# Performance work log

Hardware: AMD Instinct MI355X
Metric: run time of the kernel (lower is better)

## Reference

```python
import jax, jax.numpy as jnp
import numpy as np

B, N, U = 8, 2048, 256
BN_EPS = 1e-3  # keras BatchNormalization default epsilon
ADJ_DENSITY = 0.008  # ~16 neighbors per node on average


def setup_inputs() -> dict:
    key = jax.random.key(0)
    ks = jax.random.split(key, 16)
    s = 0.05  # weight scale ('random_normal' init is small-stddev in keras)
    x = jax.random.normal(ks[0], (B, N, U), jnp.float32)
    # sparse binary adjacency stored dense (per-sample SpMM pattern)
    adj = (jax.random.uniform(ks[1], (B, N, N)) < ADJ_DENSITY).astype(jnp.float32)
    nodal_mask = jnp.ones((B, N), jnp.float32)
    return {
        'x': x, 'adj': adj, 'nodal_mask': nodal_mask,
        'W_lin': jax.random.normal(ks[2], (U, U)) * s, 'b_lin': jnp.zeros((U,)),
        'Wq_mp': jax.random.normal(ks[3], (3, U, U)) * s, 'bq_mp': jnp.zeros((3, U)),
        'Wk_mp': jax.random.normal(ks[4], (3, U, U)) * s, 'bk_mp': jnp.zeros((3, U)),
        'Wv_mp': jax.random.normal(ks[5], (3, U, U)) * s, 'bv_mp': jnp.zeros((3, U)),
        'Wk_att': jax.random.normal(ks[6], (U, U)) * s,
        'Wv_att': jax.random.normal(ks[7], (U, U)) * s,
        'Wq_att': jax.random.normal(ks[8], (U, U)) * s,
        'Wo_att': jax.random.normal(ks[9], (U, U)) * s,
        'bn_gamma': jnp.ones((U,)), 'bn_beta': jnp.zeros((U,)),
        'bn_mean': jnp.zeros((U,)), 'bn_var': jnp.ones((U,)),
        'W_proj': jax.random.normal(ks[10], (U, U)) * s, 'b_proj': jnp.zeros((U,)),
        'W_res': jax.random.normal(ks[11], (U, U)) * s, 'b_res': jnp.zeros((U,)),
    }


def _dympn(x, adj, Ws, bs, mask):
    # 3 message-passing layers, each applied K_l=2 times (inference value)
    for i in range(3):
        for _ in range(2):
            xn = jnp.einsum('bmn,bnd->bmd', adj, x)  # batched SpMM (graph_conv mode)
            x = jax.nn.silu(jnp.einsum('bmd,de->bme', xn, Ws[i]) + bs[i])
    return x * mask[:, :, None]


def reference(x, adj, nodal_mask, W_lin, b_lin, Wq_mp, bq_mp, Wk_mp, bk_mp,
              Wv_mp, bv_mp, Wk_att, Wv_att, Wq_att, Wo_att,
              bn_gamma, bn_beta, bn_mean, bn_var, W_proj, b_proj, W_res, b_res):
    initial_x = x
    adj = jax.lax.stop_gradient(adj)
    h = jnp.einsum('bnd,de->bne', x, W_lin) + b_lin
    q = _dympn(h, adj, Wq_mp, bq_mp, nodal_mask)
    k = _dympn(h, adj, Wk_mp, bk_mp, nodal_mask)
    v = _dympn(h, adj, Wv_mp, bv_mp, nodal_mask)
    # linear attention
    m = nodal_mask[:, :, None]
    pk = jax.nn.silu(jnp.einsum('bnd,de->bne', k, Wk_att) * m)
    pv = jnp.einsum('bnd,de->bne', v, Wv_att) * m
    pq = jnp.einsum('bnd,de->bne', q, Wq_att)
    kv = jnp.einsum('bnd,bne->bde', pk, pv)       # [B,U,U]
    attn = jnp.einsum('bnd,bde->bne', pq, kv)
    attn = jnp.einsum('bnd,de->bne', attn, Wo_att)
    # batch norm (inference: moving stats) over last axis
    y = attn + initial_x
    y = bn_gamma * (y - bn_mean) * jax.lax.rsqrt(bn_var + BN_EPS) + bn_beta
    out = jax.nn.silu(jnp.einsum('bnd,de->bne', y, W_proj) + b_proj)
    out = out + jnp.einsum('bnd,de->bne', initial_x, W_res) + b_res
    out = out * nodal_mask[:, :, None]
    return out
```

## Files before the change

kernel.cpp:

```cpp
#include <hip/hip_runtime.h>
#include <stdint.h>

#define NB 8
#define NN 2048
#define NU 256
#define CAP 64
#define BNEPS 0.001f

typedef __attribute__((ext_vector_type(8))) short short8;
typedef __attribute__((ext_vector_type(4))) float floatx4;
typedef unsigned short u16;
typedef unsigned int u32;

__device__ __forceinline__ float bf2f(u16 u) {
  union { u32 i; float f; } c; c.i = ((u32)u) << 16; return c.f;
}
__device__ __forceinline__ u16 f2bf(float f) {
  union { float f; u32 i; } c; c.f = f;
  return (u16)((c.i + 0x7fffu + ((c.i >> 16) & 1u)) >> 16);
}
__device__ __forceinline__ void splitbf(float a, u16& h, u16& l) {
  h = f2bf(a);
  l = f2bf(a - bf2f(h));
}

enum : unsigned {
  F_BIAS = 2u, F_SILU = 4u, F_MASKPRE = 8u, F_MASKPOST = 16u,
  F_ADDX = 32u, F_BN = 64u, F_ADDT = 128u, F_BPERMAT = 512u,
  F_TPLANES = 1024u, F_OUTHL = 2048u
};

#define TP_MAT 524288
#define TP_LO  4194304
#define MSZ ((size_t)NN * NU)

__global__ __launch_bounds__(256) void build_nbr_k(
    const float* __restrict__ adj, int* __restrict__ cnt, int* __restrict__ idx)
{
  int row = blockIdx.x;
  const float* base = adj + (size_t)row * NN;
  __shared__ int c;
  if (threadIdx.x == 0) c = 0;
  __syncthreads();
#pragma unroll
  for (int j = 0; j < 8; j++) {
    int n = j * 256 + threadIdx.x;
    if (base[n] != 0.f) {
      int p = atomicAdd(&c, 1);
      if (p < CAP) idx[(size_t)row * CAP + p] = n;
    }
  }
  __syncthreads();
  if (threadIdx.x == 0) cnt[row] = (c < CAP ? c : CAP);
}

struct WPtrs { const float* p[16]; };

__global__ __launch_bounds__(256) void conv_w_k(WPtrs wp, u16* __restrict__ dst)
{
  int gid = blockIdx.x * 256 + threadIdx.x;
  int mat = gid >> 13;
  int rem = gid & 8191;
  int kb = rem >> 10;
  int n = (rem >> 2) & 255;
  int slot = rem & 3;
  int qv = (slot - (n >> 1)) & 3;
  int k0 = kb * 32 + qv * 8;
  const float* W = wp.p[mat];
  u32 oh[4], ol[4];
#pragma unroll
  for (int t2 = 0; t2 < 4; t2++) {
    float f0 = W[(size_t)(k0 + 2 * t2) * 256 + n];
    float f1 = W[(size_t)(k0 + 2 * t2 + 1) * 256 + n];
    u16 h0, l0, h1, l1;
    splitbf(f0, h0, l0);
    splitbf(f1, h1, l1);
    oh[t2] = (u32)h0 | ((u32)h1 << 16);
    ol[t2] = (u32)l0 | ((u32)l1 << 16);
  }
  uint4 qh; qh.x = oh[0]; qh.y = oh[1]; qh.z = oh[2]; qh.w = oh[3];
  uint4 ql; ql.x = ol[0]; ql.y = ol[1]; ql.z = ol[2]; ql.w = ol[3];
  *(uint4*)(dst + (size_t)gid * 8) = qh;
  *(uint4*)(dst + 1048576 + (size_t)gid * 8) = ql;
}

__global__ __launch_bounds__(256) void conv_x_k(
    const float* __restrict__ x, u16* __restrict__ dst, size_t oLo)
{
  size_t i = ((size_t)blockIdx.x * 256 + threadIdx.x) * 4;
  float4 v = *(const float4*)(x + i);
  u16 h0, l0, h1, l1, h2, l2, h3, l3;
  splitbf(v.x, h0, l0); splitbf(v.y, h1, l1);
  splitbf(v.z, h2, l2); splitbf(v.w, h3, l3);
  uint2 H; H.x = (u32)h0 | ((u32)h1 << 16); H.y = (u32)h2 | ((u32)h3 << 16);
  uint2 L; L.x = (u32)l0 | ((u32)l1 << 16); L.y = (u32)l2 | ((u32)l3 << 16);
  *(uint2*)(dst + i) = H;
  *(uint2*)(dst + oLo + i) = L;
}

template <unsigned F>
__device__ __forceinline__ void gemm_epi(
    floatx4 (&acc)[4][2], int b, int bm, int w, int m16, int q,
    const float* __restrict__ bias, const float* __restrict__ mask,
    const float* __restrict__ xf32,
    const float* __restrict__ gma, const float* __restrict__ bta,
    const float* __restrict__ bmu, const float* __restrict__ bvr,
    const float* __restrict__ addt, void* __restrict__ outp, size_t oLo)
{
#pragma unroll
  for (int mt = 0; mt < 4; mt++) {
    if (F & F_TPLANES) {
      u16* oh = (u16*)outp + (size_t)b * TP_MAT;
      u16* ol = oh + TP_LO;
      int gr0 = bm + mt * 16 + q * 4;
#pragma unroll
      for (int nt = 0; nt < 2; nt++) {
        int col = w * 32 + nt * 16 + m16;
        u16 hh[4], ll[4];
#pragma unroll
        for (int r = 0; r < 4; r++) {
          float t2 = acc[mt][nt][r];
          float mv = mask[b * NN + gr0 + r];
          if (F & F_MASKPRE) t2 *= mv;
          if (F & F_SILU) t2 = t2 / (1.f + __expf(-t2));
          if (F & F_MASKPOST) t2 *= mv;
          splitbf(t2, hh[r], ll[r]);
        }
        uint2 H2, L2v;
        H2.x = (u32)hh[0] | ((u32)hh[1] << 16);
        H2.y = (u32)hh[2] | ((u32)hh[3] << 16);
        L2v.x = (u32)ll[0] | ((u32)ll[1] << 16);
        L2v.y = (u32)ll[2] | ((u32)ll[3] << 16);
        *(uint2*)(oh + (size_t)col * 2048 + gr0) = H2;
        *(uint2*)(ol + (size_t)col * 2048 + gr0) = L2v;
      }
    } else {
#pragma unroll
      for (int r = 0; r < 4; r++) {
        int gr = bm + mt * 16 + q * 4 + r;
        float mval = 1.f;
        if (F & (F_MASKPRE | F_MASKPOST)) mval = mask[b * NN + gr];
#pragma unroll
        for (int nt = 0; nt < 2; nt++) {
          int col = w * 32 + nt * 16 + m16;
          float t2 = acc[mt][nt][r];
          if (F & F_BIAS) t2 += bias[col];
          if (F & F_MASKPRE) t2 *= mval;
          if (F & F_SILU) t2 = t2 / (1.f + __expf(-t2));
          if (F & F_ADDX) t2 += xf32[((size_t)b * NN + gr) * NU + col];
          if (F & F_BN) t2 = gma[col] * (t2 - bmu[col]) * rsqrtf(bvr[col] + BNEPS) + bta[col];
          if (F & F_ADDT) t2 += addt[((size_t)b * NN + gr) * NU + col];
          if (F & F_MASKPOST) t2 *= mval;
          size_t o = ((size_t)b * NN + gr) * NU + col;
          if (F & F_OUTHL) {
            u16 h0, l0;
            splitbf(t2, h0, l0);
            ((u16*)outp)[o] = h0;
            ((u16*)outp)[o + oLo] = l0;
          } else {
            ((float*)outp)[o] = t2;
          }
        }
      }
    }
  }
}

template <int NG, unsigned F0, unsigned F1, unsigned F2>
__global__ __launch_bounds__(512, 4) void gemm_k(
    const u16* __restrict__ A0, const u16* __restrict__ A1, const u16* __restrict__ A2,
    size_t aLo,
    const u16* __restrict__ W0, const u16* __restrict__ W1, const u16* __restrict__ W2,
    size_t wLo,
    const float* __restrict__ b0, const float* __restrict__ b1, const float* __restrict__ b2,
    const float* __restrict__ mask,
    const float* __restrict__ xf32,
    const float* __restrict__ gma, const float* __restrict__ bta,
    const float* __restrict__ bmu, const float* __restrict__ bvr,
    const float* __restrict__ addt,
    void* __restrict__ o0, void* __restrict__ o1, void* __restrict__ o2,
    size_t oLo)
{
  const int tid = threadIdx.x;
  const int id = blockIdx.x;
  const int xcd = id & 7;
  const int t = id >> 3;
  const int chain = (NG == 1) ? 0 : (t % NG);
  const int xt = (NG == 1) ? t : (t / NG);
  const int b = xcd;
  const int bm = xt * 64;

  __shared__ alignas(16) u16 Ah[64 * 264];
  __shared__ alignas(16) u16 Al[64 * 264];

  const u16* Abase = (chain == 0) ? A0 : (chain == 1 ? A1 : A2);
  const u16* Wsel = (chain == 0) ? W0 : (chain == 1 ? W1 : W2);
  if (F0 & F_BPERMAT) Wsel = W0 + (size_t)b * 65536;
  const u16* Whi = Wsel;
  const u16* Wlo = Whi + wLo;
  const u16* Ahp = Abase + (size_t)b * MSZ;
  const u16* Alp = Ahp + aLo;

#pragma unroll
  for (int s = tid; s < 1024; s += 512) {
    int r = s >> 4;
    int c = (s & 15) << 4;
    size_t ao = (size_t)(bm + r) * 256 + c;
    *(uint4*)&Ah[r * 264 + c] = *(const uint4*)(Ahp + ao);
    *(uint4*)&Ah[r * 264 + c + 8] = *(const uint4*)(Ahp + ao + 8);
    *(uint4*)&Al[r * 264 + c] = *(const uint4*)(Alp + ao);
    *(uint4*)&Al[r * 264 + c + 8] = *(const uint4*)(Alp + ao + 8);
  }
  __syncthreads();

  const int lane = tid & 63;
  const int w = tid >> 6;
  const int m16 = lane & 15;
  const int q = lane >> 4;

  floatx4 acc[4][2];
#pragma unroll
  for (int i = 0; i < 4; i++)
#pragma unroll
    for (int j = 0; j < 2; j++) acc[i][j] = (floatx4){0.f, 0.f, 0.f, 0.f};

#pragma unroll
  for (int kk = 0; kk < 8; kk++) {
    short8 bh[2], bl2[2];
#pragma unroll
    for (int nt = 0; nt < 2; nt++) {
      int n = w * 32 + nt * 16 + m16;
      size_t off = (size_t)kk * 8192 + (size_t)n * 32 + (size_t)(((q + (n >> 1)) & 3) * 8);
      bh[nt] = *(const short8*)(Whi + off);
      bl2[nt] = *(const short8*)(Wlo + off);
    }
#pragma unroll
    for (int mt = 0; mt < 4; mt++) {
      int row = mt * 16 + m16;
      short8 ah = *(const short8*)&Ah[row * 264 + kk * 32 + q * 8];
      short8 al2 = *(const short8*)&Al[row * 264 + kk * 32 + q * 8];
#pragma unroll
      for (int nt = 0; nt < 2; nt++) {
        acc[mt][nt] = __builtin_amdgcn_mfma_f32_16x16x32_bf16(ah, bh[nt], acc[mt][nt], 0, 0, 0);
        acc[mt][nt] = __builtin_amdgcn_mfma_f32_16x16x32_bf16(al2, bh[nt], acc[mt][nt], 0, 0, 0);
        acc[mt][nt] = __builtin_amdgcn_mfma_f32_16x16x32_bf16(ah, bl2[nt], acc[mt][nt], 0, 0, 0);
      }
    }
  }

  if (NG == 1 || chain == 0)
    gemm_epi<F0>(acc, b, bm, w, m16, q, b0, mask, xf32, gma, bta, bmu, bvr, addt, o0, oLo);
  else if (chain == 1)
    gemm_epi<F1>(acc, b, bm, w, m16, q, b1, mask, xf32, gma, bta, bmu, bvr, addt, o1, oLo);
  else
    gemm_epi<F2>(acc, b, bm, w, m16, q, b2, mask, xf32, gma, bta, bmu, bvr, addt, o2, oLo);
}

template <unsigned F>
__global__ __launch_bounds__(256, 8) void agg_k(
    const float* __restrict__ g, u16* __restrict__ xo, size_t oLo,
    const float* __restrict__ bq, const float* __restrict__ bk, const float* __restrict__ bv,
    const float* __restrict__ mask,
    const int* __restrict__ ncnt, const int* __restrict__ nidx)
{
  int id = blockIdx.x;
  int c3 = id >> 12;
  int sub = id & 4095;
  int b = sub & 7;
  int rg = sub >> 3;
  int tid = threadIdx.x;
  int w = tid >> 6;
  int l = tid & 63;
  int row = rg * 4 + w;
  int rowid = b * NN + row;
  const float* __restrict__ gm = g + ((size_t)c3 * 8 + b) * MSZ;
  const float* bias = (c3 == 0) ? bq : (c3 == 1 ? bk : bv);
  int cnt = ncnt[rowid];
  const int* __restrict__ ip = nidx + (size_t)rowid * CAP;
  int c = l * 4;
  float4 a; a.x = a.y = a.z = a.w = 0.f;
  int e = 0;
  for (; e + 4 <= cnt; e += 4) {
    int4 i4 = *(const int4*)(ip + e);
    float4 v0 = *(const float4*)(gm + ((size_t)i4.x << 8) + c);
    float4 v1 = *(const float4*)(gm + ((size_t)i4.y << 8) + c);
    float4 v2 = *(const float4*)(gm + ((size_t)i4.z << 8) + c);
    float4 v3 = *(const float4*)(gm + ((size_t)i4.w << 8) + c);
    a.x += v0.x + v1.x + v2.x + v3.x;
    a.y += v0.y + v1.y + v2.y + v3.y;
    a.z += v0.z + v1.z + v2.z + v3.z;
    a.w += v0.w + v1.w + v2.w + v3.w;
  }
  for (; e < cnt; e++) {
    float4 v = *(const float4*)(gm + ((size_t)ip[e] << 8) + c);
    a.x += v.x; a.y += v.y; a.z += v.z; a.w += v.w;
  }
  float4 bb = *(const float4*)(bias + c);
  float o[4] = {a.x + bb.x, a.y + bb.y, a.z + bb.z, a.w + bb.w};
  float mv = (F & F_MASKPOST) ? mask[rowid] : 1.f;
  u16 hh[4], ll[4];
#pragma unroll
  for (int j = 0; j < 4; j++) {
    float t = o[j];
    if (F & F_SILU) t = t / (1.f + __expf(-t));
    if (F & F_MASKPOST) t *= mv;
    splitbf(t, hh[j], ll[j]);
  }
  uint2 H; H.x = (u32)hh[0] | ((u32)hh[1] << 16); H.y = (u32)hh[2] | ((u32)hh[3] << 16);
  uint2 L; L.x = (u32)ll[0] | ((u32)ll[1] << 16); L.y = (u32)ll[2] | ((u32)ll[3] << 16);
  size_t o0 = ((size_t)c3 * 8 + b) * MSZ + ((size_t)row << 8) + c;
  *(uint2*)(xo + o0) = H;
  *(uint2*)(xo + oLo + o0) = L;
}

__global__ __launch_bounds__(256, 2) void kv_k(
    const u16* __restrict__ pkT, const u16* __restrict__ pvT, float* __restrict__ part)
{
  int et = blockIdx.x * 128;
  int dt = blockIdx.y * 128;
  int z = blockIdx.z;
  int b = z & 7;
  int p = z >> 3;
  int tid = threadIdx.x;
  int lane = tid & 63, w = tid >> 6;
  int m16 = lane & 15, q = lane >> 4;

  const u16* pkh = pkT + (size_t)b * TP_MAT;
  const u16* pkl = pkh + TP_LO;
  const u16* pvh = pvT + (size_t)b * TP_MAT;
  const u16* pvl = pvh + TP_LO;

  int d_base = dt + (w >> 1) * 64 + m16;
  int e_base = et + (w & 1) * 64 + m16;

  floatx4 acc[4][4];
#pragma unroll
  for (int i = 0; i < 4; i++)
#pragma unroll
    for (int j = 0; j < 4; j++) acc[i][j] = (floatx4){0.f, 0.f, 0.f, 0.f};

#pragma unroll
  for (int kt = 0; kt < 8; kt++) {
    int kc = p * 256 + kt * 32 + q * 8;
    short8 ah[4], al[4], bh[4], bl[4];
#pragma unroll
    for (int mt = 0; mt < 4; mt++) {
      size_t o = (size_t)(d_base + mt * 16) * 2048 + kc;
      ah[mt] = *(const short8*)(pkh + o);
      al[mt] = *(const short8*)(pkl + o);
    }
#pragma unroll
    for (int nt = 0; nt < 4; nt++) {
      size_t o = (size_t)(e_base + nt * 16) * 2048 + kc;
      bh[nt] = *(const short8*)(pvh + o);
      bl[nt] = *(const short8*)(pvl + o);
    }
#pragma unroll
    for (int mt = 0; mt < 4; mt++)
#pragma unroll
      for (int nt = 0; nt < 4; nt++) {
        acc[mt][nt] = __builtin_amdgcn_mfma_f32_16x16x32_bf16(ah[mt], bh[nt], acc[mt][nt], 0, 0, 0);
        acc[mt][nt] = __builtin_amdgcn_mfma_f32_16x16x32_bf16(al[mt], bh[nt], acc[mt][nt], 0, 0, 0);
        acc[mt][nt] = __builtin_amdgcn_mfma_f32_16x16x32_bf16(ah[mt], bl[nt], acc[mt][nt], 0, 0, 0);
      }
  }

#pragma unroll
  for (int mt = 0; mt < 4; mt++)
#pragma unroll
    for (int r = 0; r < 4; r++) {
      int d = dt + (w >> 1) * 64 + mt * 16 + q * 4 + r;
#pragma unroll
      for (int nt = 0; nt < 4; nt++) {
        int e = et + (w & 1) * 64 + nt * 16 + m16;
        part[(size_t)z * 65536 + (size_t)d * 256 + e] = acc[mt][nt][r];
      }
    }
}

__global__ __launch_bounds__(256) void kv_conv_k(const float* __restrict__ part, u16* __restrict__ dst)
{
  int gid = blockIdx.x * 256 + threadIdx.x;
  int b = gid >> 13;
  int rem = gid & 8191;
  int kb = rem >> 10;
  int e = (rem >> 2) & 255;
  int slot = rem & 3;
  int qv = (slot - (e >> 1)) & 3;
  int d0 = kb * 32 + qv * 8;
  const float* src = part + (size_t)b * 65536 + (size_t)d0 * 256 + e;
  u32 oh[4], ol[4];
#pragma unroll
  for (int t2 = 0; t2 < 4; t2++) {
    float s0 = 0.f, s1 = 0.f;
#pragma unroll
    for (int pp = 0; pp < 8; pp++) {
      const float* sp = src + (size_t)pp * 524288 + t2 * 512;
      s0 += sp[0];
      s1 += sp[256];
    }
    u16 h0, l0, h1, l1;
    splitbf(s0, h0, l0);
    splitbf(s1, h1, l1);
    oh[t2] = (u32)h0 | ((u32)h1 << 16);
    ol[t2] = (u32)l0 | ((u32)l1 << 16);
  }
  uint4 qh; qh.x = oh[0]; qh.y = oh[1]; qh.z = oh[2]; qh.w = oh[3];
  uint4 ql; ql.x = ol[0]; ql.y = ol[1]; ql.z = ol[2]; ql.w = ol[3];
  *(uint4*)(dst + (size_t)gid * 8) = qh;
  *(uint4*)(dst + 524288 + (size_t)gid * 8) = ql;
}

extern "C" void kernel_launch(void* const* d_in, const int* in_sizes, int n_in,
                              void* d_out, int out_size, void* d_ws, size_t ws_size,
                              hipStream_t stream)
{
  const float* x = (const float*)d_in[0];
  const float* adj = (const float*)d_in[1];
  const float* mask = (const float*)d_in[2];
  const float* W_lin = (const float*)d_in[3];
  const float* b_lin = (const float*)d_in[4];
  const float* Wq_mp = (const float*)d_in[5];
  const float* bq_mp = (const float*)d_in[6];
  const float* Wk_mp = (const float*)d_in[7];
  const float* bk_mp = (const float*)d_in[8];
  const float* Wv_mp = (const float*)d_in[9];
  const float* bv_mp = (const float*)d_in[10];
  const float* Wk_att = (const float*)d_in[11];
  const float* Wv_att = (const float*)d_in[12];
  const float* Wq_att = (const float*)d_in[13];
  const float* Wo_att = (const float*)d_in[14];
  const float* bn_gamma = (const float*)d_in[15];
  const float* bn_beta = (const float*)d_in[16];
  const float* bn_mean = (const float*)d_in[17];
  const float* bn_var = (const float*)d_in[18];
  const float* W_proj = (const float*)d_in[19];
  const float* b_proj = (const float*)d_in[20];
  const float* W_res = (const float*)d_in[21];
  const float* b_res = (const float*)d_in[22];

  char* ws = (char*)d_ws;
  int* CNT    = (int*)(ws + 0);
  int* IDX    = (int*)(ws + (1ull << 20));
  u16* WSZ    = (u16*)(ws + (5ull << 20));
  u16* KVS    = (u16*)(ws + (9ull << 20));
  float* KVP  = (float*)(ws + (11ull << 20));
  u16* XHL    = (u16*)(ws + (27ull << 20));
  u16* HHL    = (u16*)(ws + (43ull << 20));
  float* G    = (float*)(ws + (59ull << 20));
  u16* XA     = (u16*)(ws + (107ull << 20));
  u16* XB     = (u16*)(ws + (155ull << 20));

  const size_t WLO = 1048576;
  const size_t KLO = 524288;
  const size_t A8  = 8 * MSZ;
  const size_t A24 = 24 * MSZ;

  u16* PQHL = HHL;
  u16* PKT = (u16*)G;
  u16* PVT = (u16*)((char*)G + (16ull << 20));
  u16* ATT = (u16*)((char*)G + (32ull << 20));
  u16* YHL = XA;
  float* TMP = (float*)((char*)XA + (16ull << 20));

  WPtrs wp;
  wp.p[0] = W_lin;
  wp.p[1] = Wq_mp; wp.p[2] = Wq_mp + 65536; wp.p[3] = Wq_mp + 131072;
  wp.p[4] = Wk_mp; wp.p[5] = Wk_mp + 65536; wp.p[6] = Wk_mp + 131072;
  wp.p[7] = Wv_mp; wp.p[8] = Wv_mp + 65536; wp.p[9] = Wv_mp + 131072;
  wp.p[10] = Wk_att; wp.p[11] = Wv_att; wp.p[12] = Wq_att; wp.p[13] = Wo_att;
  wp.p[14] = W_proj; wp.p[15] = W_res;
  conv_w_k<<<512, 256, 0, stream>>>(wp, WSZ);
  conv_x_k<<<4096, 256, 0, stream>>>(x, XHL, A8);
  build_nbr_k<<<NB * NN, 256, 0, stream>>>(adj, CNT, IDX);

  gemm_k<1, F_BIAS | F_OUTHL, 0u, 0u><<<256, 512, 0, stream>>>(
      XHL, XHL, XHL, A8, WSZ, WSZ, WSZ, WLO,
      b_lin, nullptr, nullptr, mask, nullptr,
      bn_gamma, bn_beta, bn_mean, bn_var, nullptr,
      HHL, nullptr, nullptr, A8);

  u16* xbufs[2] = {XA, XB};
  for (int s = 0; s < 6; s++) {
    int i = s >> 1;
    const u16* Wq_s = WSZ + (size_t)(1 + i) * 65536;
    const u16* Wk_s = WSZ + (size_t)(4 + i) * 65536;
    const u16* Wv_s = WSZ + (size_t)(7 + i) * 65536;
    u16* inb = (s == 0) ? HHL : xbufs[(s + 1) & 1];
    size_t aLo = (s == 0) ? A8 : A24;
    const u16* Aq = inb;
    const u16* Ak = (s == 0) ? inb : inb + 8 * MSZ;
    const u16* Av = (s == 0) ? inb : inb + 16 * MSZ;
    u16* ob = xbufs[s & 1];
    gemm_k<3, 0u, 0u, 0u><<<768, 512, 0, stream>>>(
        Aq, Ak, Av, aLo, Wq_s, Wk_s, Wv_s, WLO,
        nullptr, nullptr, nullptr, mask, nullptr,
        bn_gamma, bn_beta, bn_mean, bn_var, nullptr,
        G, G + 8 * MSZ, G + 16 * MSZ, 0);
    const float* bq = bq_mp + i * 256;
    const float* bk = bk_mp + i * 256;
    const float* bv = bv_mp + i * 256;
    if (s == 5)
      agg_k<F_BIAS | F_SILU | F_MASKPOST><<<12288, 256, 0, stream>>>(
          G, ob, A24, bq, bk, bv, mask, CNT, IDX);
    else
      agg_k<F_BIAS | F_SILU><<<12288, 256, 0, stream>>>(
          G, ob, A24, bq, bk, bv, mask, CNT, IDX);
  }

  gemm_k<3, F_OUTHL, F_SILU | F_MASKPRE | F_TPLANES, F_MASKPOST | F_TPLANES>
      <<<768, 512, 0, stream>>>(
      XB, XB + 8 * MSZ, XB + 16 * MSZ, A24,
      WSZ + (size_t)12 * 65536, WSZ + (size_t)10 * 65536, WSZ + (size_t)11 * 65536, WLO,
      nullptr, nullptr, nullptr, mask, nullptr,
      bn_gamma, bn_beta, bn_mean, bn_var, nullptr,
      PQHL, PKT, PVT, A8);

  kv_k<<<dim3(2, 2, 64), 256, 0, stream>>>(PKT, PVT, KVP);
  kv_conv_k<<<256, 256, 0, stream>>>(KVP, KVS);

  gemm_k<1, F_BPERMAT | F_OUTHL, 0u, 0u><<<256, 512, 0, stream>>>(
      PQHL, PQHL, PQHL, A8, KVS, KVS, KVS, KLO,
      nullptr, nullptr, nullptr, mask, nullptr,
      bn_gamma, bn_beta, bn_mean, bn_var, nullptr,
      ATT, nullptr, nullptr, A8);

  gemm_k<1, F_ADDX | F_BN | F_OUTHL, 0u, 0u><<<256, 512, 0, stream>>>(
      ATT, ATT, ATT, A8,
      WSZ + (size_t)13 * 65536, nullptr, nullptr, WLO,
      nullptr, nullptr, nullptr, mask, x,
      bn_gamma, bn_beta, bn_mean, bn_var, nullptr,
      YHL, nullptr, nullptr, A8);

  gemm_k<1, F_BIAS, 0u, 0u><<<256, 512, 0, stream>>>(
      XHL, XHL, XHL, A8,
      WSZ + (size_t)15 * 65536, nullptr, nullptr, WLO,
      b_res, nullptr, nullptr, mask, nullptr,
      bn_gamma, bn_beta, bn_mean, bn_var, nullptr,
      TMP, nullptr, nullptr, 0);

  gemm_k<1, F_BIAS | F_SILU | F_ADDT | F_MASKPOST, 0u, 0u><<<256, 512, 0, stream>>>(
      YHL, YHL, YHL, A8,
      WSZ + (size_t)14 * 65536, nullptr, nullptr, WLO,
      b_proj, nullptr, nullptr, mask, nullptr,
      bn_gamma, bn_beta, bn_mean, bn_var, TMP,
      d_out, nullptr, nullptr, 0);

  (void)in_sizes; (void)n_in; (void)out_size; (void)ws_size;
}
```

Before: 793.1 us.

## Fuse sparse neighbor aggregation into following GEMM prologue and merge setup kernels

Removes the separate agg_k kernel. Each GEMM now gathers the neighbor rows of the previous GEMM's fp32 output, adds bias, applies SiLU and mask, splits to bf16 hi/lo, and writes the result straight into shared memory as its A tile. This avoids writing and re-reading the intermediate bf16 hi/lo planes and saves six launches. The three setup kernels become one prologue kernel, and the chain index mapping changes to t>>5 so blocks of the same chain are grouped. The cost is that the gather now sits on the GEMM's critical path with fewer threads per row, which may leave the load latency exposed.

```diff
diff --git a/kernel.cpp b/kernel.cpp
--- a/kernel.cpp
+++ b/kernel.cpp
@@ -34,68 +34,67 @@
 #define TP_LO  4194304
 #define MSZ ((size_t)NN * NU)
 
-__global__ __launch_bounds__(256) void build_nbr_k(
+struct WPtrs { const float* p[16]; };
+
+__global__ __launch_bounds__(256) void prologue_k(
+    WPtrs wp, u16* __restrict__ wdst,
+    const float* __restrict__ x, u16* __restrict__ xdst, size_t xLo,
     const float* __restrict__ adj, int* __restrict__ cnt, int* __restrict__ idx)
 {
-  int row = blockIdx.x;
-  const float* base = adj + (size_t)row * NN;
-  __shared__ int c;
-  if (threadIdx.x == 0) c = 0;
-  __syncthreads();
-#pragma unroll
-  for (int j = 0; j < 8; j++) {
-    int n = j * 256 + threadIdx.x;
-    if (base[n] != 0.f) {
-      int p = atomicAdd(&c, 1);
-      if (p < CAP) idx[(size_t)row * CAP + p] = n;
-    }
-  }
-  __syncthreads();
-  if (threadIdx.x == 0) cnt[row] = (c < CAP ? c : CAP);
-}
-
-struct WPtrs { const float* p[16]; };
-
-__global__ __launch_bounds__(256) void conv_w_k(WPtrs wp, u16* __restrict__ dst)
-{
-  int gid = blockIdx.x * 256 + threadIdx.x;
-  int mat = gid >> 13;
-  int rem = gid & 8191;
-  int kb = rem >> 10;
-  int n = (rem >> 2) & 255;
-  int slot = rem & 3;
-  int qv = (slot - (n >> 1)) & 3;
-  int k0 = kb * 32 + qv * 8;
-  const float* W = wp.p[mat];
-  u32 oh[4], ol[4];
-#pragma unroll
-  for (int t2 = 0; t2 < 4; t2++) {
-    float f0 = W[(size_t)(k0 + 2 * t2) * 256 + n];
-    float f1 = W[(size_t)(k0 + 2 * t2 + 1) * 256 + n];
-    u16 h0, l0, h1, l1;
-    splitbf(f0, h0, l0);
-    splitbf(f1, h1, l1);
-    oh[t2] = (u32)h0 | ((u32)h1 << 16);
-    ol[t2] = (u32)l0 | ((u32)l1 << 16);
-  }
-  uint4 qh; qh.x = oh[0]; qh.y = oh[1]; qh.z = oh[2]; qh.w = oh[3];
-  uint4 ql; ql.x = ol[0]; ql.y = ol[1]; ql.z = ol[2]; ql.w = ol[3];
-  *(uint4*)(dst + (size_t)gid * 8) = qh;
-  *(uint4*)(dst + 1048576 + (size_t)gid * 8) = ql;
-}
-
-__global__ __launch_bounds__(256) void conv_x_k(
-    const float* __restrict__ x, u16* __restrict__ dst, size_t oLo)
-{
-  size_t i = ((size_t)blockIdx.x * 256 + threadIdx.x) * 4;
-  float4 v = *(const float4*)(x + i);
-  u16 h0, l0, h1, l1, h2, l2, h3, l3;
-  splitbf(v.x, h0, l0); splitbf(v.y, h1, l1);
-  splitbf(v.z, h2, l2); splitbf(v.w, h3, l3);
-  uint2 H; H.x = (u32)h0 | ((u32)h1 << 16); H.y = (u32)h2 | ((u32)h3 << 16);
-  uint2 L; L.x = (u32)l0 | ((u32)l1 << 16); L.y = (u32)l2 | ((u32)l3 << 16);
-  *(uint2*)(dst + i) = H;
-  *(uint2*)(dst + oLo + i) = L;
+  int bid = blockIdx.x;
+  int tid = threadIdx.x;
+  __shared__ int c0;
+  if (bid < 512) {
+    int gid = bid * 256 + tid;
+    int mat = gid >> 13;
+    int rem = gid & 8191;
+    int kb = rem >> 10;
+    int n = (rem >> 2) & 255;
+    int slot = rem & 3;
+    int qv = (slot - (n >> 1)) & 3;
+    int k0 = kb * 32 + qv * 8;
+    const float* W = wp.p[mat];
+    u32 oh[4], ol[4];
+#pragma unroll
+    for (int t2 = 0; t2 < 4; t2++) {
+      float f0 = W[(size_t)(k0 + 2 * t2) * 256 + n];
+      float f1 = W[(size_t)(k0 + 2 * t2 + 1) * 256 + n];
+      u16 h0, l0, h1, l1;
+      splitbf(f0, h0, l0);
+      splitbf(f1, h1, l1);
+      oh[t2] = (u32)h0 | ((u32)h1 << 16);
+      ol[t2] = (u32)l0 | ((u32)l1 << 16);
+    }
+    uint4 qh; qh.x = oh[0]; qh.y = oh[1]; qh.z = oh[2]; qh.w = oh[3];
+    uint4 ql; ql.x = ol[0]; ql.y = ol[1]; ql.z = ol[2]; ql.w = ol[3];
+    *(uint4*)(wdst + (size_t)gid * 8) = qh;
+    *(uint4*)(wdst + 1048576 + (size_t)gid * 8) = ql;
+  } else if (bid < 4608) {
+    size_t i = ((size_t)(bid - 512) * 256 + tid) * 4;
+    float4 v = *(const float4*)(x + i);
+    u16 h0, l0, h1, l1, h2, l2, h3, l3;
+    splitbf(v.x, h0, l0); splitbf(v.y, h1, l1);
+    splitbf(v.z, h2, l2); splitbf(v.w, h3, l3);
+    uint2 H; H.x = (u32)h0 | ((u32)h1 << 16); H.y = (u32)h2 | ((u32)h3 << 16);
+    uint2 L; L.x = (u32)l0 | ((u32)l1 << 16); L.y = (u32)l2 | ((u32)l3 << 16);
+    *(uint2*)(xdst + i) = H;
+    *(uint2*)(xdst + xLo + i) = L;
+  } else {
+    int row = bid - 4608;
+    const float* base = adj + (size_t)row * NN;
+    if (tid == 0) c0 = 0;
+    __syncthreads();
+#pragma unroll
+    for (int j = 0; j < 8; j++) {
+      int n = j * 256 + tid;
+      if (base[n] != 0.f) {
+        int p = atomicAdd(&c0, 1);
+        if (p < CAP) idx[(size_t)row * CAP + p] = n;
+      }
+    }
+    __syncthreads();
+    if (tid == 0) cnt[row] = (c0 < CAP ? c0 : CAP);
+  }
 }
 
 template <unsigned F>
@@ -166,7 +165,7 @@
   }
 }
 
-template <int NG, unsigned F0, unsigned F1, unsigned F2>
+template <int NG, unsigned SF, unsigned F0, unsigned F1, unsigned F2>
 __global__ __launch_bounds__(512, 4) void gemm_k(
     const u16* __restrict__ A0, const u16* __restrict__ A1, const u16* __restrict__ A2,
     size_t aLo,
@@ -179,37 +178,88 @@
     const float* __restrict__ bmu, const float* __restrict__ bvr,
     const float* __restrict__ addt,
     void* __restrict__ o0, void* __restrict__ o1, void* __restrict__ o2,
-    size_t oLo)
+    size_t oLo,
+    const float* __restrict__ gsrc,
+    const float* __restrict__ sb0, const float* __restrict__ sb1, const float* __restrict__ sb2,
+    const int* __restrict__ ncnt, const int* __restrict__ nidx)
 {
   const int tid = threadIdx.x;
   const int id = blockIdx.x;
   const int xcd = id & 7;
   const int t = id >> 3;
-  const int chain = (NG == 1) ? 0 : (t % NG);
-  const int xt = (NG == 1) ? t : (t / NG);
+  const int chain = (NG == 1) ? 0 : (t >> 5);
+  const int xt = (NG == 1) ? t : (t & 31);
   const int b = xcd;
   const int bm = xt * 64;
 
   __shared__ alignas(16) u16 Ah[64 * 264];
   __shared__ alignas(16) u16 Al[64 * 264];
 
-  const u16* Abase = (chain == 0) ? A0 : (chain == 1 ? A1 : A2);
   const u16* Wsel = (chain == 0) ? W0 : (chain == 1 ? W1 : W2);
   if (F0 & F_BPERMAT) Wsel = W0 + (size_t)b * 65536;
   const u16* Whi = Wsel;
   const u16* Wlo = Whi + wLo;
-  const u16* Ahp = Abase + (size_t)b * MSZ;
-  const u16* Alp = Ahp + aLo;
-
-#pragma unroll
-  for (int s = tid; s < 1024; s += 512) {
-    int r = s >> 4;
-    int c = (s & 15) << 4;
-    size_t ao = (size_t)(bm + r) * 256 + c;
-    *(uint4*)&Ah[r * 264 + c] = *(const uint4*)(Ahp + ao);
-    *(uint4*)&Ah[r * 264 + c + 8] = *(const uint4*)(Ahp + ao + 8);
-    *(uint4*)&Al[r * 264 + c] = *(const uint4*)(Alp + ao);
-    *(uint4*)&Al[r * 264 + c + 8] = *(const uint4*)(Alp + ao + 8);
+
+  if constexpr (SF != 0u) {
+    const int l = tid & 63;
+    const int wv = tid >> 6;
+    const float* __restrict__ gm = gsrc + ((size_t)chain * 8 + b) * MSZ;
+    const float* sb = (chain == 0) ? sb0 : (chain == 1 ? sb1 : sb2);
+    const int c = l * 4;
+    float4 bb = *(const float4*)(sb + c);
+#pragma unroll 1
+    for (int i = 0; i < 8; i++) {
+      const int r = wv * 8 + i;
+      const int gr = bm + r;
+      const int rowid = b * NN + gr;
+      const int cnt = ncnt[rowid];
+      const int* __restrict__ ip = nidx + (size_t)rowid * CAP;
+      float4 a; a.x = a.y = a.z = a.w = 0.f;
+      int e = 0;
+      for (; e + 4 <= cnt; e += 4) {
+        int4 i4 = *(const int4*)(ip + e);
+        float4 v0 = *(const float4*)(gm + ((size_t)i4.x << 8) + c);
+        float4 v1 = *(const float4*)(gm + ((size_t)i4.y << 8) + c);
+        float4 v2 = *(const float4*)(gm + ((size_t)i4.z << 8) + c);
+        float4 v3 = *(const float4*)(gm + ((size_t)i4.w << 8) + c);
+        a.x += v0.x + v1.x + v2.x + v3.x;
+        a.y += v0.y + v1.y + v2.y + v3.y;
+        a.z += v0.z + v1.z + v2.z + v3.z;
+        a.w += v0.w + v1.w + v2.w + v3.w;
+      }
+      for (; e < cnt; e++) {
+        float4 v = *(const float4*)(gm + ((size_t)ip[e] << 8) + c);
+        a.x += v.x; a.y += v.y; a.z += v.z; a.w += v.w;
+      }
+      float ov[4] = {a.x + bb.x, a.y + bb.y, a.z + bb.z, a.w + bb.w};
+      float mv = (SF & F_MASKPOST) ? mask[rowid] : 1.f;
+      u16 hh[4], ll[4];
+#pragma unroll
+      for (int j = 0; j < 4; j++) {
+        float t2 = ov[j];
+        if (SF & F_SILU) t2 = t2 / (1.f + __expf(-t2));
+        if (SF & F_MASKPOST) t2 *= mv;
+        splitbf(t2, hh[j], ll[j]);
+      }
+      uint2 H; H.x = (u32)hh[0] | ((u32)hh[1] << 16); H.y = (u32)hh[2] | ((u32)hh[3] << 16);
+      uint2 L; L.x = (u32)ll[0] | ((u32)ll[1] << 16); L.y = (u32)ll[2] | ((u32)ll[3] << 16);
+      *(uint2*)&Ah[r * 264 + c] = H;
+      *(uint2*)&Al[r * 264 + c] = L;
+    }
+  } else {
+    const u16* Abase = (chain == 0) ? A0 : (chain == 1 ? A1 : A2);
+    const u16* Ahp = Abase + (size_t)b * MSZ;
+    const u16* Alp = Ahp + aLo;
+#pragma unroll
+    for (int s = tid; s < 1024; s += 512) {
+      int r = s >> 4;
+      int c = (s & 15) << 4;
+      size_t ao = (size_t)(bm + r) * 256 + c;
+      *(uint4*)&Ah[r * 264 + c] = *(const uint4*)(Ahp + ao);
+      *(uint4*)&Ah[r * 264 + c + 8] = *(const uint4*)(Ahp + ao + 8);
+      *(uint4*)&Al[r * 264 + c] = *(const uint4*)(Alp + ao);
+      *(uint4*)&Al[r * 264 + c + 8] = *(const uint4*)(Alp + ao + 8);
+    }
   }
   __syncthreads();
 
@@ -254,63 +304,6 @@
     gemm_epi<F1>(acc, b, bm, w, m16, q, b1, mask, xf32, gma, bta, bmu, bvr, addt, o1, oLo);
   else
     gemm_epi<F2>(acc, b, bm, w, m16, q, b2, mask, xf32, gma, bta, bmu, bvr, addt, o2, oLo);
-}
-
-template <unsigned F>
-__global__ __launch_bounds__(256, 8) void agg_k(
-    const float* __restrict__ g, u16* __restrict__ xo, size_t oLo,
-    const float* __restrict__ bq, const float* __restrict__ bk, const float* __restrict__ bv,
-    const float* __restrict__ mask,
-    const int* __restrict__ ncnt, const int* __restrict__ nidx)
-{
-  int id = blockIdx.x;
-  int c3 = id >> 12;
-  int sub = id & 4095;
-  int b = sub & 7;
-  int rg = sub >> 3;
-  int tid = threadIdx.x;
-  int w = tid >> 6;
-  int l = tid & 63;
-  int row = rg * 4 + w;
-  int rowid = b * NN + row;
-  const float* __restrict__ gm = g + ((size_t)c3 * 8 + b) * MSZ;
-  const float* bias = (c3 == 0) ? bq : (c3 == 1 ? bk : bv);
-  int cnt = ncnt[rowid];
-  const int* __restrict__ ip = nidx + (size_t)rowid * CAP;
-  int c = l * 4;
-  float4 a; a.x = a.y = a.z = a.w = 0.f;
-  int e = 0;
-  for (; e + 4 <= cnt; e += 4) {
-    int4 i4 = *(const int4*)(ip + e);
-    float4 v0 = *(const float4*)(gm + ((size_t)i4.x << 8) + c);
-    float4 v1 = *(const float4*)(gm + ((size_t)i4.y << 8) + c);
-    float4 v2 = *(const float4*)(gm + ((size_t)i4.z << 8) + c);
-    float4 v3 = *(const float4*)(gm + ((size_t)i4.w << 8) + c);
-    a.x += v0.x + v1.x + v2.x + v3.x;
-    a.y += v0.y + v1.y + v2.y + v3.y;
-    a.z += v0.z + v1.z + v2.z + v3.z;
-    a.w += v0.w + v1.w + v2.w + v3.w;
-  }
-  for (; e < cnt; e++) {
-    float4 v = *(const float4*)(gm + ((size_t)ip[e] << 8) + c);
-    a.x += v.x; a.y += v.y; a.z += v.z; a.w += v.w;
-  }
-  float4 bb = *(const float4*)(bias + c);
-  float o[4] = {a.x + bb.x, a.y + bb.y, a.z + bb.z, a.w + bb.w};
-  float mv = (F & F_MASKPOST) ? mask[rowid] : 1.f;
-  u16 hh[4], ll[4];
-#pragma unroll
-  for (int j = 0; j < 4; j++) {
-    float t = o[j];
-    if (F & F_SILU) t = t / (1.f + __expf(-t));
-    if (F & F_MASKPOST) t *= mv;
-    splitbf(t, hh[j], ll[j]);
-  }
-  uint2 H; H.x = (u32)hh[0] | ((u32)hh[1] << 16); H.y = (u32)hh[2] | ((u32)hh[3] << 16);
-  uint2 L; L.x = (u32)ll[0] | ((u32)ll[1] << 16); L.y = (u32)ll[2] | ((u32)ll[3] << 16);
-  size_t o0 = ((size_t)c3 * 8 + b) * MSZ + ((size_t)row << 8) + c;
-  *(uint2*)(xo + o0) = H;
-  *(uint2*)(xo + oLo + o0) = L;
 }
 
 __global__ __launch_bounds__(256, 2) void kv_k(
@@ -447,21 +440,19 @@
   float* KVP  = (float*)(ws + (11ull << 20));
   u16* XHL    = (u16*)(ws + (27ull << 20));
   u16* HHL    = (u16*)(ws + (43ull << 20));
-  float* G    = (float*)(ws + (59ull << 20));
-  u16* XA     = (u16*)(ws + (107ull << 20));
-  u16* XB     = (u16*)(ws + (155ull << 20));
+  float* GA   = (float*)(ws + (59ull << 20));
+  float* GB   = (float*)(ws + (107ull << 20));
+  u16* PKT    = (u16*)(ws + (155ull << 20));
+  u16* PVT    = (u16*)(ws + (171ull << 20));
+  u16* ATT    = (u16*)(ws + (187ull << 20));
+  u16* YHL    = (u16*)(ws + (203ull << 20));
+  float* TMP  = (float*)(ws + (219ull << 20));
 
   const size_t WLO = 1048576;
   const size_t KLO = 524288;
   const size_t A8  = 8 * MSZ;
-  const size_t A24 = 24 * MSZ;
 
   u16* PQHL = HHL;
-  u16* PKT = (u16*)G;
-  u16* PVT = (u16*)((char*)G + (16ull << 20));
-  u16* ATT = (u16*)((char*)G + (32ull << 20));
-  u16* YHL = XA;
-  float* TMP = (float*)((char*)XA + (16ull << 20));
 
   WPtrs wp;
   wp.p[0] = W_lin;
@@ -470,81 +461,81 @@
   wp.p[7] = Wv_mp; wp.p[8] = Wv_mp + 65536; wp.p[9] = Wv_mp + 131072;
   wp.p[10] = Wk_att; wp.p[11] = Wv_att; wp.p[12] = Wq_att; wp.p[13] = Wo_att;
   wp.p[14] = W_proj; wp.p[15] = W_res;
-  conv_w_k<<<512, 256, 0, stream>>>(wp, WSZ);
-  conv_x_k<<<4096, 256, 0, stream>>>(x, XHL, A8);
-  build_nbr_k<<<NB * NN, 256, 0, stream>>>(adj, CNT, IDX);
-
-  gemm_k<1, F_BIAS | F_OUTHL, 0u, 0u><<<256, 512, 0, stream>>>(
+  prologue_k<<<20992, 256, 0, stream>>>(wp, WSZ, x, XHL, A8, adj, CNT, IDX);
+
+  gemm_k<1, 0u, F_BIAS | F_OUTHL, 0u, 0u><<<256, 512, 0, stream>>>(
       XHL, XHL, XHL, A8, WSZ, WSZ, WSZ, WLO,
       b_lin, nullptr, nullptr, mask, nullptr,
       bn_gamma, bn_beta, bn_mean, bn_var, nullptr,
-      HHL, nullptr, nullptr, A8);
-
-  u16* xbufs[2] = {XA, XB};
-  for (int s = 0; s < 6; s++) {
-    int i = s >> 1;
-    const u16* Wq_s = WSZ + (size_t)(1 + i) * 65536;
-    const u16* Wk_s = WSZ + (size_t)(4 + i) * 65536;
-    const u16* Wv_s = WSZ + (size_t)(7 + i) * 65536;
-    u16* inb = (s == 0) ? HHL : xbufs[(s + 1) & 1];
-    size_t aLo = (s == 0) ? A8 : A24;
-    const u16* Aq = inb;
-    const u16* Ak = (s == 0) ? inb : inb + 8 * MSZ;
-    const u16* Av = (s == 0) ? inb : inb + 16 * MSZ;
-    u16* ob = xbufs[s & 1];
-    gemm_k<3, 0u, 0u, 0u><<<768, 512, 0, stream>>>(
-        Aq, Ak, Av, aLo, Wq_s, Wk_s, Wv_s, WLO,
+      HHL, nullptr, nullptr, A8,
+      nullptr, nullptr, nullptr, nullptr, CNT, IDX);
+
+  gemm_k<3, 0u, 0u, 0u, 0u><<<768, 512, 0, stream>>>(
+      HHL, HHL, HHL, A8,
+      WSZ + (size_t)1 * 65536, WSZ + (size_t)4 * 65536, WSZ + (size_t)7 * 65536, WLO,
+      nullptr, nullptr, nullptr, mask, nullptr,
+      bn_gamma, bn_beta, bn_mean, bn_var, nullptr,
+      GA, GA + 8 * MSZ, GA + 16 * MSZ, 0,
+      nullptr, nullptr, nullptr, nullptr, CNT, IDX);
+
+  for (int s = 1; s < 6; s++) {
+    int iw = s >> 1;
+    int ib = (s - 1) >> 1;
+    float* Gin = (s & 1) ? GA : GB;
+    float* Gout = (s & 1) ? GB : GA;
+    gemm_k<3, F_BIAS | F_SILU, 0u, 0u, 0u><<<768, 512, 0, stream>>>(
+        nullptr, nullptr, nullptr, 0,
+        WSZ + (size_t)(1 + iw) * 65536, WSZ + (size_t)(4 + iw) * 65536,
+        WSZ + (size_t)(7 + iw) * 65536, WLO,
         nullptr, nullptr, nullptr, mask, nullptr,
         bn_gamma, bn_beta, bn_mean, bn_var, nullptr,
-        G, G + 8 * MSZ, G + 16 * MSZ, 0);
-    const float* bq = bq_mp + i * 256;
-    const float* bk = bk_mp + i * 256;
-    const float* bv = bv_mp + i * 256;
-    if (s == 5)
-      agg_k<F_BIAS | F_SILU | F_MASKPOST><<<12288, 256, 0, stream>>>(
-          G, ob, A24, bq, bk, bv, mask, CNT, IDX);
-    else
-      agg_k<F_BIAS | F_SILU><<<12288, 256, 0, stream>>>(
-          G, ob, A24, bq, bk, bv, mask, CNT, IDX);
-  }
-
-  gemm_k<3, F_OUTHL, F_SILU | F_MASKPRE | F_TPLANES, F_MASKPOST | F_TPLANES>
+        Gout, Gout + 8 * MSZ, Gout + 16 * MSZ, 0,
+        Gin, bq_mp + ib * 256, bk_mp + ib * 256, bv_mp + ib * 256, CNT, IDX);
+  }
+
+  gemm_k<3, F_BIAS | F_SILU | F_MASKPOST,
+         F_OUTHL, F_SILU | F_MASKPRE | F_TPLANES, F_MASKPOST | F_TPLANES>
       <<<768, 512, 0, stream>>>(
-      XB, XB + 8 * MSZ, XB + 16 * MSZ, A24,
+      nullptr, nullptr, nullptr, 0,
       WSZ + (size_t)12 * 65536, WSZ + (size_t)10 * 65536, WSZ + (size_t)11 * 65536, WLO,
       nullptr, nullptr, nullptr, mask, nullptr,
       bn_gamma, bn_beta, bn_mean, bn_var, nullptr,
-      PQHL, PKT, PVT, A8);
+      PQHL, PKT, PVT, A8,
+      GB, bq_mp + 512, bk_mp + 512, bv_mp + 512, CNT, IDX);
 
   kv_k<<<dim3(2, 2, 64), 256, 0, stream>>>(PKT, PVT, KVP);
   kv_conv_k<<<256, 256, 0, stream>>>(KVP, KVS);
 
-  gemm_k<1, F_BPERMAT | F_OUTHL, 0u, 0u><<<256, 512, 0, stream>>>(
+  gemm_k<1, 0u, F_BPERMAT | F_OUTHL, 0u, 0u><<<256, 512, 0, stream>>>(
       PQHL, PQHL, PQHL, A8, KVS, KVS, KVS, KLO,
       nullptr, nullptr, nullptr, mask, nullptr,
       bn_gamma, bn_beta, bn_mean, bn_var, nullptr,
-      ATT, nullptr, nullptr, A8);
-
-  gemm_k<1, F_ADDX | F_BN | F_OUTHL, 0u, 0u><<<256, 512, 0, stream>>>(
+      ATT, nullptr, nullptr, A8,
+      nullptr, nullptr, nullptr, nullptr, CNT, IDX);
+
+  gemm_k<1, 0u, F_ADDX | F_BN | F_OUTHL, 0u, 0u><<<256, 512, 0, stream>>>(
       ATT, ATT, ATT, A8,
       WSZ + (size_t)13 * 65536, nullptr, nullptr, WLO,
       nullptr, nullptr, nullptr, mask, x,
       bn_gamma, bn_beta, bn_mean, bn_var, nullptr,
-      YHL, nullptr, nullptr, A8);
-
-  gemm_k<1, F_BIAS, 0u, 0u><<<256, 512, 0, stream>>>(
+      YHL, nullptr, nullptr, A8,
+      nullptr, nullptr, nullptr, nullptr, CNT, IDX);
+
+  gemm_k<1, 0u, F_BIAS, 0u, 0u><<<256, 512, 0, stream>>>(
       XHL, XHL, XHL, A8,
       WSZ + (size_t)15 * 65536, nullptr, nullptr, WLO,
       b_res, nullptr, nullptr, mask, nullptr,
       bn_gamma, bn_beta, bn_mean, bn_var, nullptr,
-      TMP, nullptr, nullptr, 0);
-
-  gemm_k<1, F_BIAS | F_SILU | F_ADDT | F_MASKPOST, 0u, 0u><<<256, 512, 0, stream>>>(
+      TMP, nullptr, nullptr, 0,
+      nullptr, nullptr, nullptr, nullptr, CNT, IDX);
+
+  gemm_k<1, 0u, F_BIAS | F_SILU | F_ADDT | F_MASKPOST, 0u, 0u><<<256, 512, 0, stream>>>(
       YHL, YHL, YHL, A8,
       WSZ + (size_t)14 * 65536, nullptr, nullptr, WLO,
       b_proj, nullptr, nullptr, mask, nullptr,
       bn_gamma, bn_beta, bn_mean, bn_var, TMP,
-      d_out, nullptr, nullptr, 0);
+      d_out, nullptr, nullptr, 0,
+      nullptr, nullptr, nullptr, nullptr, CNT, IDX);
 
   (void)in_sizes; (void)n_in; (void)out_size; (void)ws_size;
 }
```

Result: slower. 840.9 us (+6.0%).
